# Kernel tuning notes

Measured on AMD Instinct MI355X. Metric: run time of the kernel, lower is better.

The kernel has to match this reference:

```python
import jax, jax.numpy as jnp
import numpy as np

D_MODEL = 2048
NUM_Q_HEADS = 32
NUM_KV_HEADS = 8
HEAD_DIM = D_MODEL // NUM_Q_HEADS  # 64
NUM_GROUPS = NUM_Q_HEADS // NUM_KV_HEADS  # 4
SCALE = float(np.sqrt(HEAD_DIM))


def setup_inputs() -> dict:
    key = jax.random.key(0)
    ks = jax.random.split(key, 5)
    B, S = 2, 2048
    std = 1.0 / np.sqrt(D_MODEL)
    return {
        "x": jax.random.normal(ks[0], (B, S, D_MODEL), dtype=jnp.float32),
        "W_q": jax.random.normal(ks[1], (D_MODEL, NUM_Q_HEADS * HEAD_DIM), dtype=jnp.float32) * std,
        "W_k": jax.random.normal(ks[2], (D_MODEL, NUM_KV_HEADS * HEAD_DIM), dtype=jnp.float32) * std,
        "W_v": jax.random.normal(ks[3], (D_MODEL, NUM_KV_HEADS * HEAD_DIM), dtype=jnp.float32) * std,
        "W_o": jax.random.normal(ks[4], (D_MODEL, D_MODEL), dtype=jnp.float32) * std,
    }


def reference(x, W_q, W_k, W_v, W_o):
    B, S, _ = x.shape
    # projections; weights stored as (in, out) so y = x @ W
    Q = (x @ W_q).reshape(B, S, NUM_Q_HEADS, HEAD_DIM).transpose(0, 2, 1, 3)   # [B,Hq,S,d]
    K = (x @ W_k).reshape(B, S, NUM_KV_HEADS, HEAD_DIM).transpose(0, 2, 1, 3)  # [B,Hkv,S,d]
    V = (x @ W_v).reshape(B, S, NUM_KV_HEADS, HEAD_DIM).transpose(0, 2, 1, 3)
    # repeat_interleave KV heads across groups (faithful to the original)
    K = jnp.repeat(K, NUM_GROUPS, axis=1)  # [B,Hq,S,d]
    V = jnp.repeat(V, NUM_GROUPS, axis=1)
    scores = jnp.einsum("bhqd,bhkd->bhqk", Q, K) / SCALE  # [B,Hq,S,S]
    attn = jax.nn.softmax(scores, axis=-1)
    out = jnp.einsum("bhqk,bhkd->bhqd", attn, V)  # [B,Hq,S,d]
    out = out.transpose(0, 2, 1, 3).reshape(B, S, D_MODEL)
    return out @ W_o
```

## Files before the change

### kernel.cpp

```cpp
#include <hip/hip_runtime.h>
#include <hip/hip_bf16.h>

#define D_MODEL 2048
#define NQH 32
#define NKVH 8
#define HD 64
#define SEQ 2048
#define BATCH 2
#define MTOT (BATCH * SEQ)

typedef __attribute__((ext_vector_type(8))) short short8;
typedef __attribute__((ext_vector_type(4))) float floatx4;
typedef __attribute__((ext_vector_type(16))) float f32x16;

#define QSCALE 0.18033688011112042f

#if __has_builtin(__builtin_amdgcn_exp2f)
#define EXP2(x) __builtin_amdgcn_exp2f(x)
#else
#define EXP2(x) exp2f(x)
#endif

static __device__ inline unsigned cvtpk(float lo, float hi) {
  unsigned r;
  asm("v_cvt_pk_bf16_f32 %0, %1, %2" : "=v"(r) : "v"(lo), "v"(hi));
  return r;
}
#define PLSWAP(a, b) asm("v_permlane32_swap_b32 %0, %1" : "+v"(a), "+v"(b))

__device__ inline void gload_lds16(const __hip_bfloat16* g, short* lds) {
  __builtin_amdgcn_global_load_lds(
      (const __attribute__((address_space(1))) void*)g,
      (__attribute__((address_space(3))) void*)lds, 16, 0, 0);
}

__global__ __launch_bounds__(256) void convx_k(const float* __restrict__ x,
                                               __hip_bfloat16* __restrict__ xb,
                                               int n4) {
  int i = blockIdx.x * 256 + threadIdx.x;
  int stride = gridDim.x * 256;
  for (; i < n4; i += stride) {
    float4 v = reinterpret_cast<const float4*>(x)[i];
    union { __hip_bfloat16 h[4]; uint2 u; } cv;
    cv.h[0] = __float2bfloat16(v.x);
    cv.h[1] = __float2bfloat16(v.y);
    cv.h[2] = __float2bfloat16(v.z);
    cv.h[3] = __float2bfloat16(v.w);
    reinterpret_cast<uint2*>(xb)[i] = cv.u;
  }
}

__global__ __launch_bounds__(256) void transw_k(const float* __restrict__ W,
                                                __hip_bfloat16* __restrict__ Wt,
                                                int Kd, int Nd) {
  __shared__ float t[32][33];
  int n0 = blockIdx.x * 32, k0 = blockIdx.y * 32;
  int tx = threadIdx.x, ty = threadIdx.y;
#pragma unroll
  for (int j = 0; j < 32; j += 8)
    t[ty + j][tx] = W[(size_t)(k0 + ty + j) * Nd + n0 + tx];
  __syncthreads();
#pragma unroll
  for (int j = 0; j < 32; j += 8)
    Wt[(size_t)(n0 + ty + j) * Kd + k0 + tx] = __float2bfloat16(t[tx][ty + j]);
}

template <int MODE>
__global__ __launch_bounds__(256) void gemm_bt_k(
    const __hip_bfloat16* __restrict__ A,
    const __hip_bfloat16* __restrict__ B0,
    const __hip_bfloat16* __restrict__ B1,
    const __hip_bfloat16* __restrict__ B2,
    float* __restrict__ Cf,
    __hip_bfloat16* __restrict__ O0,
    __hip_bfloat16* __restrict__ O1,
    __hip_bfloat16* __restrict__ O2) {
  constexpr int Kd = D_MODEL;
  __shared__ short As[128 * 32];
  __shared__ short Bs[128 * 32];

  const int tid = threadIdx.x;
  const int m0 = blockIdx.y * 128;
  const int n0 = blockIdx.x * 128;

  const __hip_bfloat16* Bt;
  if (MODE == 0) {
    Bt = B0 + (size_t)n0 * Kd;
  } else {
    if (n0 < 2048) Bt = B0 + (size_t)n0 * Kd;
    else if (n0 < 2560) Bt = B1 + (size_t)(n0 - 2048) * Kd;
    else Bt = B2 + (size_t)(n0 - 2560) * Kd;
  }
  const __hip_bfloat16* Ab = A + (size_t)m0 * Kd;

  const int w = tid >> 6, l = tid & 63;
  const int wr = w >> 1, wc = w & 1;
  const int lc = l & 15, l4 = l >> 4;

  const int srow = w * 32 + (l >> 2);
  const int scol = (l & 3) * 8;
  const __hip_bfloat16* ga = Ab + (size_t)srow * Kd + scol;
  const __hip_bfloat16* gb = Bt + (size_t)srow * Kd + scol;
  short* la0 = &As[(w * 32) * 32];
  short* la1 = &As[(w * 32 + 16) * 32];
  short* lb0 = &Bs[(w * 32) * 32];
  short* lb1 = &Bs[(w * 32 + 16) * 32];

  floatx4 acc[4][4] = {};

  for (int kt = 0; kt < Kd; kt += 32) {
    gload_lds16(ga + kt, la0);
    gload_lds16(ga + (size_t)16 * Kd + kt, la1);
    gload_lds16(gb + kt, lb0);
    gload_lds16(gb + (size_t)16 * Kd + kt, lb1);
    __syncthreads();

    short8 af[4], bf[4];
#pragma unroll
    for (int mi = 0; mi < 4; ++mi)
      af[mi] = *reinterpret_cast<const short8*>(&As[(wr * 64 + mi * 16 + lc) * 32 + l4 * 8]);
#pragma unroll
    for (int ni = 0; ni < 4; ++ni)
      bf[ni] = *reinterpret_cast<const short8*>(&Bs[(wc * 64 + ni * 16 + lc) * 32 + l4 * 8]);
#pragma unroll
    for (int mi = 0; mi < 4; ++mi)
#pragma unroll
      for (int ni = 0; ni < 4; ++ni)
        acc[mi][ni] = __builtin_amdgcn_mfma_f32_16x16x32_bf16(af[mi], bf[ni], acc[mi][ni], 0, 0, 0);
    __syncthreads();
  }

#pragma unroll
  for (int mi = 0; mi < 4; ++mi)
#pragma unroll
    for (int ni = 0; ni < 4; ++ni)
#pragma unroll
      for (int i = 0; i < 4; ++i) {
        int m = m0 + wr * 64 + mi * 16 + l4 * 4 + i;
        int ncol = n0 + wc * 64 + ni * 16 + lc;
        float v = acc[mi][ni][i];
        if (MODE == 0) {
          Cf[(size_t)m * 2048 + ncol] = v;
        } else {
          int bb = m >> 11, s = m & 2047;
          if (ncol < 2048) {
            int hh = ncol >> 6, dd = ncol & 63;
            O0[(((size_t)bb * NQH + hh) * SEQ + s) * HD + dd] = __float2bfloat16(v * QSCALE);
          } else if (ncol < 2560) {
            int c2 = ncol - 2048;
            int hh = c2 >> 6, dd = c2 & 63;
            O1[(((size_t)bb * NKVH + hh) * SEQ + s) * HD + dd] = __float2bfloat16(v);
          } else {
            int c2 = ncol - 2560;
            int hh = c2 >> 6, dd = c2 & 63;
            O2[(((size_t)bb * NKVH + hh) * HD + dd) * SEQ + s] = __float2bfloat16(v);
          }
        }
      }
}

__global__ __launch_bounds__(256, 4) void attn_k(const __hip_bfloat16* __restrict__ Qb,
                                                 const __hip_bfloat16* __restrict__ Kb,
                                                 const __hip_bfloat16* __restrict__ Vtb,
                                                 __hip_bfloat16* __restrict__ Ao) {
  __shared__ short Ks[2][64 * 64];
  __shared__ short Vs[2][64 * 64];
  __shared__ float Ls[4][32];

  const int bid = blockIdx.x;
  const int xcd = bid & 7, j = bid >> 3;
  const int g = xcd * 2 + (j >> 6), wv = j & 63;
  const int b = g >> 3, kh = g & 7;
  const int h = kh * 4 + (wv >> 4), qt = wv & 15;

  const int tid = threadIdx.x, w = tid >> 6, l = tid & 63;
  const int q5 = l & 31, hl = l >> 5;

  const __hip_bfloat16* Qp = Qb + (((size_t)b * NQH + h) * SEQ + qt * 128 + w * 32) * HD;
  const __hip_bfloat16* Kp = Kb + ((size_t)b * NKVH + kh) * SEQ * HD;
  const __hip_bfloat16* Vp = Vtb + ((size_t)b * NKVH + kh) * HD * SEQ;

  short8 qf[4];
#pragma unroll
  for (int ks = 0; ks < 4; ++ks)
    qf[ks] = *reinterpret_cast<const short8*>(Qp + (size_t)q5 * HD + ks * 16 + hl * 8);

  f32x16 acc0 = {}, acc1 = {};
  float lsum = 0.f;

  const int rg = l >> 3;
  const int cc = (l & 7) ^ (rg & 7);
  const __hip_bfloat16* sK = Kp + (size_t)(16 * w + rg) * HD + cc * 8;
  const __hip_bfloat16* sV = Vp + (size_t)(16 * w + rg) * SEQ + cc * 8;

  int fo[4];
#pragma unroll
  for (int jj = 0; jj < 4; ++jj)
    fo[jj] = q5 * 64 + (((jj * 2 + hl) ^ (q5 & 7)) * 8);

  gload_lds16(sK, &Ks[0][1024 * w]);
  gload_lds16(sK + 8 * HD, &Ks[0][1024 * w + 512]);
  gload_lds16(sV, &Vs[0][1024 * w]);
  gload_lds16(sV + 8 * (size_t)SEQ, &Vs[0][1024 * w + 512]);
  sK += 64 * HD;
  sV += 64;
  __syncthreads();

  for (int kb = 0; kb < SEQ / 64; ++kb) {
    const short* Kt = Ks[kb & 1];
    const short* Vt = Vs[kb & 1];

    if (kb + 1 < SEQ / 64) {
      short* Kn = Ks[(kb & 1) ^ 1];
      short* Vn = Vs[(kb & 1) ^ 1];
      gload_lds16(sK, &Kn[1024 * w]);
      gload_lds16(sK + 8 * HD, &Kn[1024 * w + 512]);
      gload_lds16(sV, &Vn[1024 * w]);
      gload_lds16(sV + 8 * (size_t)SEQ, &Vn[1024 * w + 512]);
      sK += 64 * HD;
      sV += 64;
    }

    short8 kf0[4], kf1[4];
#pragma unroll
    for (int ks = 0; ks < 4; ++ks) {
      kf0[ks] = *reinterpret_cast<const short8*>(&Kt[fo[ks]]);
      kf1[ks] = *reinterpret_cast<const short8*>(&Kt[fo[ks] + 2048]);
    }
    f32x16 st0 = {}, st1 = {};
    __builtin_amdgcn_s_setprio(1);
#pragma unroll
    for (int ks = 0; ks < 4; ++ks) {
      st0 = __builtin_amdgcn_mfma_f32_32x32x16_bf16(kf0[ks], qf[ks], st0, 0, 0, 0);
      st1 = __builtin_amdgcn_mfma_f32_32x32x16_bf16(kf1[ks], qf[ks], st1, 0, 0, 0);
    }
    __builtin_amdgcn_s_setprio(0);

    float ps = 0.f;
    unsigned u0[8], u1[8];
#pragma unroll
    for (int jj = 0; jj < 8; ++jj) {
      float e0 = EXP2(st0[2 * jj]), e1 = EXP2(st0[2 * jj + 1]);
      float f0 = EXP2(st1[2 * jj]), f1 = EXP2(st1[2 * jj + 1]);
      ps += (e0 + e1) + (f0 + f1);
      u0[jj] = cvtpk(e0, e1);
      u1[jj] = cvtpk(f0, f1);
    }
    lsum += ps;

    short8 vf0[4], vf1[4];
#pragma unroll
    for (int t = 0; t < 4; ++t) {
      vf0[t] = *reinterpret_cast<const short8*>(&Vt[fo[t]]);
      vf1[t] = *reinterpret_cast<const short8*>(&Vt[fo[t] + 2048]);
    }

    PLSWAP(u0[0], u0[2]); PLSWAP(u0[1], u0[3]);
    PLSWAP(u0[4], u0[6]); PLSWAP(u0[5], u0[7]);
    PLSWAP(u1[0], u1[2]); PLSWAP(u1[1], u1[3]);
    PLSWAP(u1[4], u1[6]); PLSWAP(u1[5], u1[7]);

    __builtin_amdgcn_s_setprio(1);
#pragma unroll
    for (int t = 0; t < 4; ++t) {
      union { unsigned w4[4]; short8 s8; } pa;
      pa.w4[0] = (t >> 1 ? u1 : u0)[(t & 1) * 4 + 0];
      pa.w4[1] = (t >> 1 ? u1 : u0)[(t & 1) * 4 + 1];
      pa.w4[2] = (t >> 1 ? u1 : u0)[(t & 1) * 4 + 2];
      pa.w4[3] = (t >> 1 ? u1 : u0)[(t & 1) * 4 + 3];
      acc0 = __builtin_amdgcn_mfma_f32_32x32x16_bf16(pa.s8, vf0[t], acc0, 0, 0, 0);
      acc1 = __builtin_amdgcn_mfma_f32_32x32x16_bf16(pa.s8, vf1[t], acc1, 0, 0, 0);
    }
    __builtin_amdgcn_s_setprio(0);
    __syncthreads();
  }

  {
    float v = lsum;
    v += __shfl_xor(v, 32);
    if (l < 32) Ls[w][l] = v;
  }
  __syncthreads();

  const size_t obase = (size_t)b * SEQ + qt * 128 + w * 32;
  float inv[16];
#pragma unroll
  for (int r = 0; r < 16; ++r)
    inv[r] = 1.0f / Ls[w][(r & 3) + 8 * (r >> 2) + 4 * hl];
#pragma unroll
  for (int r = 0; r < 16; ++r) {
    int q = (r & 3) + 8 * (r >> 2) + 4 * hl;
    Ao[(obase + q) * D_MODEL + h * HD + q5] = __float2bfloat16(acc0[r] * inv[r]);
    Ao[(obase + q) * D_MODEL + h * HD + 32 + q5] = __float2bfloat16(acc1[r] * inv[r]);
  }
}

extern "C" void kernel_launch(void* const* d_in, const int* in_sizes, int n_in,
                              void* d_out, int out_size, void* d_ws, size_t ws_size,
                              hipStream_t stream) {
  const float* x  = (const float*)d_in[0];
  const float* Wq = (const float*)d_in[1];
  const float* Wk = (const float*)d_in[2];
  const float* Wv = (const float*)d_in[3];
  const float* Wo = (const float*)d_in[4];
  float* out = (float*)d_out;

  __hip_bfloat16* p = (__hip_bfloat16*)d_ws;
  __hip_bfloat16* xb  = p;
  __hip_bfloat16* Wqt = xb  + (size_t)MTOT * D_MODEL;
  __hip_bfloat16* Wkt = Wqt + (size_t)D_MODEL * D_MODEL;
  __hip_bfloat16* Wvt = Wkt + (size_t)512 * D_MODEL;
  __hip_bfloat16* Wot = Wvt + (size_t)512 * D_MODEL;
  __hip_bfloat16* Qb  = Wot + (size_t)D_MODEL * D_MODEL;
  __hip_bfloat16* Kb  = Qb  + (size_t)MTOT * D_MODEL;
  __hip_bfloat16* Vtb = Kb  + (size_t)BATCH * NKVH * SEQ * HD;
  __hip_bfloat16* Ab  = Vtb + (size_t)BATCH * NKVH * SEQ * HD;

  convx_k<<<2048, 256, 0, stream>>>(x, xb, MTOT * D_MODEL / 4);
  transw_k<<<dim3(D_MODEL / 32, D_MODEL / 32), dim3(32, 8), 0, stream>>>(Wq, Wqt, D_MODEL, D_MODEL);
  transw_k<<<dim3(512 / 32, D_MODEL / 32), dim3(32, 8), 0, stream>>>(Wk, Wkt, D_MODEL, 512);
  transw_k<<<dim3(512 / 32, D_MODEL / 32), dim3(32, 8), 0, stream>>>(Wv, Wvt, D_MODEL, 512);
  transw_k<<<dim3(D_MODEL / 32, D_MODEL / 32), dim3(32, 8), 0, stream>>>(Wo, Wot, D_MODEL, D_MODEL);

  gemm_bt_k<1><<<dim3(24, MTOT / 128), 256, 0, stream>>>(xb, Wqt, Wkt, Wvt,
                                                         nullptr, Qb, Kb, Vtb);
  attn_k<<<dim3(1024), 256, 0, stream>>>(Qb, Kb, Vtb, Ab);
  gemm_bt_k<0><<<dim3(D_MODEL / 128, MTOT / 128), 256, 0, stream>>>(Ab, Wot, nullptr, nullptr,
                                                                    out, nullptr, nullptr, nullptr);
}
```

Before: 232.0 us.

## Rewrite projection GEMMs as 8-wave triple-buffered pipelined kernel with swizzled LDS

Replaces the 128x128 single-buffered GEMM with a 256x128 tile, 512-thread kernel that triple-buffers K=64 slices in LDS. Global loads for slice t+2 are issued in two halves interleaved with two MFMA phases, using s_setprio and explicit waitcnt/barriers. LDS columns are XOR-swizzled to avoid bank conflicts, and an XCD-aware block index remap improves L2 locality. The aim is to hide global memory latency and raise MFMA utilisation in both projection GEMMs. In exchange it uses about 144KB of LDS for one block per CU and depends on fragile manual synchronisation.

```diff
diff --git a/kernel.cpp b/kernel.cpp
--- a/kernel.cpp
+++ b/kernel.cpp
@@ -66,7 +66,7 @@
 }
 
 template <int MODE>
-__global__ __launch_bounds__(256) void gemm_bt_k(
+__global__ __launch_bounds__(512, 1) void gemm8p_k(
     const __hip_bfloat16* __restrict__ A,
     const __hip_bfloat16* __restrict__ B0,
     const __hip_bfloat16* __restrict__ B1,
@@ -76,12 +76,17 @@
     __hip_bfloat16* __restrict__ O1,
     __hip_bfloat16* __restrict__ O2) {
   constexpr int Kd = D_MODEL;
-  __shared__ short As[128 * 32];
-  __shared__ short Bs[128 * 32];
-
-  const int tid = threadIdx.x;
-  const int m0 = blockIdx.y * 128;
-  const int n0 = blockIdx.x * 128;
+  constexpr int NT = Kd / 64;
+  constexpr int NB = (MODE == 0) ? 16 : 24;
+  constexpr int NWG = 16 * NB;
+
+  __shared__ short Asb[3][16384];
+  __shared__ short Bsb[3][8192];
+
+  const int bid = blockIdx.x;
+  const int swz = (bid & 7) * (NWG / 8) + (bid >> 3);
+  const int by = swz / NB, bx = swz % NB;
+  const int m0 = by * 256, n0 = bx * 128;
 
   const __hip_bfloat16* Bt;
   if (MODE == 0) {
@@ -93,70 +98,125 @@
   }
   const __hip_bfloat16* Ab = A + (size_t)m0 * Kd;
 
-  const int w = tid >> 6, l = tid & 63;
-  const int wr = w >> 1, wc = w & 1;
+  const int tid = threadIdx.x, w = tid >> 6, l = tid & 63;
+  const int wm = w >> 2, wn = w & 3;
   const int lc = l & 15, l4 = l >> 4;
 
-  const int srow = w * 32 + (l >> 2);
-  const int scol = (l & 3) * 8;
-  const __hip_bfloat16* ga = Ab + (size_t)srow * Kd + scol;
-  const __hip_bfloat16* gb = Bt + (size_t)srow * Kd + scol;
-  short* la0 = &As[(w * 32) * 32];
-  short* la1 = &As[(w * 32 + 16) * 32];
-  short* lb0 = &Bs[(w * 32) * 32];
-  short* lb1 = &Bs[(w * 32 + 16) * 32];
-
-  floatx4 acc[4][4] = {};
-
-  for (int kt = 0; kt < Kd; kt += 32) {
-    gload_lds16(ga + kt, la0);
-    gload_lds16(ga + (size_t)16 * Kd + kt, la1);
-    gload_lds16(gb + kt, lb0);
-    gload_lds16(gb + (size_t)16 * Kd + kt, lb1);
-    __syncthreads();
-
-    short8 af[4], bf[4];
-#pragma unroll
-    for (int mi = 0; mi < 4; ++mi)
-      af[mi] = *reinterpret_cast<const short8*>(&As[(wr * 64 + mi * 16 + lc) * 32 + l4 * 8]);
-#pragma unroll
-    for (int ni = 0; ni < 4; ++ni)
-      bf[ni] = *reinterpret_cast<const short8*>(&Bs[(wc * 64 + ni * 16 + lc) * 32 + l4 * 8]);
-#pragma unroll
-    for (int mi = 0; mi < 4; ++mi)
-#pragma unroll
-      for (int ni = 0; ni < 4; ++ni)
-        acc[mi][ni] = __builtin_amdgcn_mfma_f32_16x16x32_bf16(af[mi], bf[ni], acc[mi][ni], 0, 0, 0);
-    __syncthreads();
-  }
-
-#pragma unroll
-  for (int mi = 0; mi < 4; ++mi)
-#pragma unroll
-    for (int ni = 0; ni < 4; ++ni)
-#pragma unroll
-      for (int i = 0; i < 4; ++i) {
-        int m = m0 + wr * 64 + mi * 16 + l4 * 4 + i;
-        int ncol = n0 + wc * 64 + ni * 16 + lc;
-        float v = acc[mi][ni][i];
-        if (MODE == 0) {
-          Cf[(size_t)m * 2048 + ncol] = v;
-        } else {
-          int bb = m >> 11, s = m & 2047;
-          if (ncol < 2048) {
-            int hh = ncol >> 6, dd = ncol & 63;
-            O0[(((size_t)bb * NQH + hh) * SEQ + s) * HD + dd] = __float2bfloat16(v * QSCALE);
-          } else if (ncol < 2560) {
-            int c2 = ncol - 2048;
-            int hh = c2 >> 6, dd = c2 & 63;
-            O1[(((size_t)bb * NKVH + hh) * SEQ + s) * HD + dd] = __float2bfloat16(v);
+  const int srow = w * 8 + (l >> 3);
+  const int scc = (l & 7) ^ (l >> 3);
+
+#define STAGE_A(L, SB, KT) \
+  gload_lds16(Ab + (size_t)((L)*64 + srow) * Kd + (KT) + scc * 8, &Asb[SB][(L)*4096 + w * 512])
+#define STAGE_B(L, SB, KT) \
+  gload_lds16(Bt + (size_t)((L)*64 + srow) * Kd + (KT) + scc * 8, &Bsb[SB][(L)*4096 + w * 512])
+
+  floatx4 acc[8][2] = {};
+
+  int cx[2];
+#pragma unroll
+  for (int kk = 0; kk < 2; ++kk) cx[kk] = (((kk * 4 + l4) ^ (lc & 7)) * 8);
+  const int abase = (wm * 128 + lc) * 64;
+  const int bbase = (wn * 32 + lc) * 64;
+
+  STAGE_A(0, 0, 0); STAGE_A(1, 0, 0); STAGE_A(2, 0, 0); STAGE_A(3, 0, 0);
+  STAGE_B(0, 0, 0); STAGE_B(1, 0, 0);
+  STAGE_A(0, 1, 64); STAGE_A(1, 1, 64); STAGE_A(2, 1, 64); STAGE_A(3, 1, 64);
+  STAGE_B(0, 1, 64); STAGE_B(1, 1, 64);
+  asm volatile("s_waitcnt vmcnt(6)" ::: "memory");
+  __builtin_amdgcn_s_barrier();
+
+  short8 af[4][2], bfr[2][2];
+
+  for (int t = 0; t < NT; ++t) {
+    const int rb = t % 3, sb = (t + 2) % 3;
+    const int ksrc = ((t + 2) % NT) * 64;
+    const short* Ar = Asb[rb];
+    const short* Br = Bsb[rb];
+
+#pragma unroll
+    for (int mi = 0; mi < 4; ++mi)
+#pragma unroll
+      for (int kk = 0; kk < 2; ++kk)
+        af[mi][kk] = *reinterpret_cast<const short8*>(&Ar[abase + mi * 1024 + cx[kk]]);
+#pragma unroll
+    for (int ni = 0; ni < 2; ++ni)
+#pragma unroll
+      for (int kk = 0; kk < 2; ++kk)
+        bfr[ni][kk] = *reinterpret_cast<const short8*>(&Br[bbase + ni * 1024 + cx[kk]]);
+
+    STAGE_A(0, sb, ksrc); STAGE_A(1, sb, ksrc); STAGE_B(0, sb, ksrc);
+
+    __builtin_amdgcn_s_barrier();
+    asm volatile("s_waitcnt lgkmcnt(0)" ::: "memory");
+    __builtin_amdgcn_sched_barrier(0);
+    __builtin_amdgcn_s_setprio(1);
+#pragma unroll
+    for (int mi = 0; mi < 4; ++mi)
+#pragma unroll
+      for (int ni = 0; ni < 2; ++ni)
+#pragma unroll
+        for (int kk = 0; kk < 2; ++kk)
+          acc[mi][ni] = __builtin_amdgcn_mfma_f32_16x16x32_bf16(
+              af[mi][kk], bfr[ni][kk], acc[mi][ni], 0, 0, 0);
+    __builtin_amdgcn_s_setprio(0);
+    __builtin_amdgcn_s_barrier();
+
+#pragma unroll
+    for (int mi = 0; mi < 4; ++mi)
+#pragma unroll
+      for (int kk = 0; kk < 2; ++kk)
+        af[mi][kk] = *reinterpret_cast<const short8*>(&Ar[abase + 4096 + mi * 1024 + cx[kk]]);
+
+    STAGE_A(2, sb, ksrc); STAGE_A(3, sb, ksrc); STAGE_B(1, sb, ksrc);
+
+    asm volatile("s_waitcnt vmcnt(6)" ::: "memory");
+    __builtin_amdgcn_s_barrier();
+    asm volatile("s_waitcnt lgkmcnt(0)" ::: "memory");
+    __builtin_amdgcn_sched_barrier(0);
+    __builtin_amdgcn_s_setprio(1);
+#pragma unroll
+    for (int mi = 0; mi < 4; ++mi)
+#pragma unroll
+      for (int ni = 0; ni < 2; ++ni)
+#pragma unroll
+        for (int kk = 0; kk < 2; ++kk)
+          acc[4 + mi][ni] = __builtin_amdgcn_mfma_f32_16x16x32_bf16(
+              af[mi][kk], bfr[ni][kk], acc[4 + mi][ni], 0, 0, 0);
+    __builtin_amdgcn_s_setprio(0);
+    __builtin_amdgcn_s_barrier();
+  }
+#undef STAGE_A
+#undef STAGE_B
+
+#pragma unroll
+  for (int qm = 0; qm < 2; ++qm)
+#pragma unroll
+    for (int mi = 0; mi < 4; ++mi)
+#pragma unroll
+      for (int ni = 0; ni < 2; ++ni)
+#pragma unroll
+        for (int i = 0; i < 4; ++i) {
+          int m = m0 + wm * 128 + qm * 64 + mi * 16 + l4 * 4 + i;
+          int ncol = n0 + wn * 32 + ni * 16 + lc;
+          float v = acc[qm * 4 + mi][ni][i];
+          if (MODE == 0) {
+            Cf[(size_t)m * 2048 + ncol] = v;
           } else {
-            int c2 = ncol - 2560;
-            int hh = c2 >> 6, dd = c2 & 63;
-            O2[(((size_t)bb * NKVH + hh) * HD + dd) * SEQ + s] = __float2bfloat16(v);
+            int bb = m >> 11, s = m & 2047;
+            if (ncol < 2048) {
+              int hh = ncol >> 6, dd = ncol & 63;
+              O0[(((size_t)bb * NQH + hh) * SEQ + s) * HD + dd] = __float2bfloat16(v * QSCALE);
+            } else if (ncol < 2560) {
+              int c2 = ncol - 2048;
+              int hh = c2 >> 6, dd = c2 & 63;
+              O1[(((size_t)bb * NKVH + hh) * SEQ + s) * HD + dd] = __float2bfloat16(v);
+            } else {
+              int c2 = ncol - 2560;
+              int hh = c2 >> 6, dd = c2 & 63;
+              O2[(((size_t)bb * NKVH + hh) * HD + dd) * SEQ + s] = __float2bfloat16(v);
+            }
           }
         }
-      }
 }
 
 __global__ __launch_bounds__(256, 4) void attn_k(const __hip_bfloat16* __restrict__ Qb,
@@ -322,9 +382,9 @@
   transw_k<<<dim3(512 / 32, D_MODEL / 32), dim3(32, 8), 0, stream>>>(Wv, Wvt, D_MODEL, 512);
   transw_k<<<dim3(D_MODEL / 32, D_MODEL / 32), dim3(32, 8), 0, stream>>>(Wo, Wot, D_MODEL, D_MODEL);
 
-  gemm_bt_k<1><<<dim3(24, MTOT / 128), 256, 0, stream>>>(xb, Wqt, Wkt, Wvt,
-                                                         nullptr, Qb, Kb, Vtb);
+  gemm8p_k<1><<<dim3(16 * 24), 512, 0, stream>>>(xb, Wqt, Wkt, Wvt,
+                                                 nullptr, Qb, Kb, Vtb);
   attn_k<<<dim3(1024), 256, 0, stream>>>(Qb, Kb, Vtb, Ab);
-  gemm_bt_k<0><<<dim3(D_MODEL / 128, MTOT / 128), 256, 0, stream>>>(Ab, Wot, nullptr, nullptr,
-                                                                    out, nullptr, nullptr, nullptr);
-}
+  gemm8p_k<0><<<dim3(16 * 16), 512, 0, stream>>>(Ab, Wot, nullptr, nullptr,
+                                                 out, nullptr, nullptr, nullptr);
+}
```

After: 233.4 us. About the same (+0.6%).
